# Kernel optimization log

Measured on AMD Instinct MI355X. Metric: run time of the kernel, lower is better.

The kernel has to match this reference:

```python
import jax, jax.numpy as jnp
import numpy as np

PARENT_LIST = [0, 0, 1, 2, 3, 4, 5, 6, 7, 8, 8, 3, 11, 12, 13, 14, 15, 15, 0, 18, 19, 20, 0, 22, 23, 24, 3]
J, D, H, L, DFF = 27, 512, 8, 6, 2048
DH = D // H
RADIUS = 0.1
B, N = 64, 2048
NEG = -1e9  # large finite negative: exp underflows to exactly 0 in fp32, grad-safe


def _topo_mask():
    m = np.full((J, J), NEG, dtype=np.float32)
    for c, p in enumerate(PARENT_LIST):
        m[c, c] = 0.0
        if c != p:
            m[c, p] = 0.0
            m[p, c] = 0.0
    return jnp.asarray(m)


def _radius_scales():
    s = np.ones(J, dtype=np.float32)
    s[[0, 1, 2, 3, 18, 22]] = 0.6
    s[[9, 10, 16, 17, 20, 21, 24, 25, 26]] = 1.5
    return jnp.asarray(s).reshape(1, J, 1)


def _ln(x, s, b):
    mu = jnp.mean(x, -1, keepdims=True)
    v = jnp.mean((x - mu) ** 2, -1, keepdims=True)
    return (x - mu) * jax.lax.rsqrt(v + 1e-5) * s + b


def _mha(q_in, k_in, v_in, qkv_w, qkv_b, out_w, out_b, add_mask):
    Bq, Q, _ = q_in.shape
    S = k_in.shape[1]
    q = (q_in @ qkv_w[:, :D] + qkv_b[:D]).reshape(Bq, Q, H, DH)
    k = (k_in @ qkv_w[:, D:2 * D] + qkv_b[D:2 * D]).reshape(Bq, S, H, DH)
    v = (v_in @ qkv_w[:, 2 * D:] + qkv_b[2 * D:]).reshape(Bq, S, H, DH)
    scores = jnp.einsum('bqhd,bkhd->bhqk', q, k) * np.float32(1.0 / np.sqrt(DH))
    attn = jax.nn.softmax(scores + add_mask, axis=-1)
    o = jnp.einsum('bhqk,bkhd->bqhd', attn, v).reshape(Bq, Q, D)
    return o @ out_w + out_b


def setup_inputs() -> dict:
    key = jax.random.key(0)
    ks = iter(jax.random.split(key, 40))
    def w(shape, scale=0.02):
        return jax.random.normal(next(ks), shape, jnp.float32) * scale
    return dict(
        x_t=jax.random.normal(next(ks), (B, J, 3), jnp.float32),
        t=jax.random.uniform(next(ks), (B, 1), jnp.float32),
        coarse_pose=jax.random.normal(next(ks), (B, J, 3), jnp.float32),
        radar_pc=jax.random.normal(next(ks), (B, N, 6), jnp.float32),
        pc_w=w((6, D)), pc_b=jnp.zeros(D),
        coarse_w=w((3, D)), coarse_b=jnp.zeros(D),
        state_w=w((3, D)), state_b=jnp.zeros(D),
        jid_emb=w((J, D), 1.0),
        dop_w1=w((1, 64)), dop_b1=jnp.zeros(64),
        dop_w2=w((64, D)), dop_b2=jnp.zeros(D),
        time_w1=w((1, D)), time_b1=jnp.zeros(D),
        time_w2=w((D, D)), time_b2=jnp.zeros(D),
        mod_w1=w((D, 2 * D)), mod_b1=jnp.zeros(2 * D),
        mod_w2=w((2 * D, 2 * D)), mod_b2=jnp.zeros(2 * D),
        diff_w=w((2 * D, D)), diff_b=jnp.zeros(D),
        vel_w=w((D, 3)), vel_b=jnp.zeros(3),
        sa_qkv_w=w((L, D, 3 * D)), sa_qkv_b=jnp.zeros((L, 3 * D)),
        sa_out_w=w((L, D, D)), sa_out_b=jnp.zeros((L, D)),
        ca_qkv_w=w((L, D, 3 * D)), ca_qkv_b=jnp.zeros((L, 3 * D)),
        ca_out_w=w((L, D, D)), ca_out_b=jnp.zeros((L, D)),
        ff1_w=w((L, D, DFF)), ff1_b=jnp.zeros((L, DFF)),
        ff2_w=w((L, DFF, D)), ff2_b=jnp.zeros((L, D)),
        ln1_s=jnp.ones((L, D)), ln1_b=jnp.zeros((L, D)),
        ln2_s=jnp.ones((L, D)), ln2_b=jnp.zeros((L, D)),
        ln3_s=jnp.ones((L, D)), ln3_b=jnp.zeros((L, D)),
    )


def reference(x_t, t, coarse_pose, radar_pc, pc_w, pc_b, coarse_w, coarse_b,
              state_w, state_b, jid_emb, dop_w1, dop_b1, dop_w2, dop_b2,
              time_w1, time_b1, time_w2, time_b2, mod_w1, mod_b1, mod_w2, mod_b2,
              diff_w, diff_b, vel_w, vel_b,
              sa_qkv_w, sa_qkv_b, sa_out_w, sa_out_b,
              ca_qkv_w, ca_qkv_b, ca_out_w, ca_out_b,
              ff1_w, ff1_b, ff2_w, ff2_b,
              ln1_s, ln1_b, ln2_s, ln2_b, ln3_s, ln3_b):
    p_idx = jnp.asarray(PARENT_LIST)
    topo = _topo_mask()          # [J,J] additive
    scales = _radius_scales()    # [1,J,1]
    pc_xyz = radar_pc[:, :, :3]
    pc_dop = radar_pc[:, :, 3:4]
    raw_memory = radar_pc @ pc_w + pc_b                               # [B,N,D]
    # euclidean distance via norm expansion (cdist p=2)
    d2 = (jnp.sum(x_t ** 2, -1)[:, :, None] + jnp.sum(pc_xyz ** 2, -1)[:, None, :]
          - 2.0 * jnp.einsum('bjc,bnc->bjn', x_t, pc_xyz))
    dist = jnp.sqrt(jnp.maximum(d2, 0.0))                             # [B,J,N]
    ar = scales * RADIUS                                              # [1,J,1]
    sig = ar / 2.0
    dw = jnp.exp(-dist ** 2 / (2.0 * sig ** 2))                       # [B,J,N]
    pi = jnp.max(dw, axis=1, keepdims=True)                           # [B,1,N]
    memory = raw_memory * jnp.swapaxes(pi, 1, 2)                      # [B,N,D]
    dop_feat = jax.nn.silu(pc_dop @ dop_w1 + dop_b1) @ dop_w2 + dop_b2
    denom = jnp.sum(dw, -1, keepdims=True) + 1e-6
    h_dop = jnp.einsum('bjn,bnd->bjd', dw, dop_feat) / denom
    h_coarse = coarse_pose @ coarse_w + coarse_b
    h_time = (jax.nn.silu(t @ time_w1 + time_b1) @ time_w2 + time_b2)[:, None, :]
    h_state = x_t @ state_w + state_b
    h_parent = h_state[:, p_idx, :]
    h_struct = jnp.concatenate([h_state, h_parent], -1) @ diff_w + diff_b
    query = h_coarse + h_time + h_dop + h_state + h_struct + jid_emb[None]
    mod = jax.nn.silu(h_state @ mod_w1 + mod_b1) @ mod_w2 + mod_b2
    shift, scale = jnp.split(mod, 2, axis=-1)
    query = query * (1.0 + scale) + shift
    # radius mask with nearest-point rescue
    smask = dist > ar
    min_idx = jnp.argmin(dist, axis=-1)                               # [B,J]
    rescue = jnp.arange(dist.shape[-1])[None, None, :] != min_idx[:, :, None]
    smask = jnp.where(jnp.all(smask, -1, keepdims=True), rescue, smask)
    mem_bias = jnp.where(smask, NEG, 0.0)[:, None, :, :]              # [B,1,J,N]
    tgt_bias = topo[None, None]                                       # [1,1,J,J]
    x = query
    for l in range(L):  # norm_first TransformerDecoderLayer, relu FFN, no dropout
        h = _ln(x, ln1_s[l], ln1_b[l])
        x = x + _mha(h, h, h, sa_qkv_w[l], sa_qkv_b[l], sa_out_w[l], sa_out_b[l], tgt_bias)
        h = _ln(x, ln2_s[l], ln2_b[l])
        x = x + _mha(h, memory, memory, ca_qkv_w[l], ca_qkv_b[l], ca_out_w[l], ca_out_b[l], mem_bias)
        h = _ln(x, ln3_s[l], ln3_b[l])
        x = x + jax.nn.relu(h @ ff1_w[l] + ff1_b[l]) @ ff2_w[l] + ff2_b[l]
    return x @ vel_w + vel_b
```

## Files before the change

kernel.cpp:

```cpp
#include <hip/hip_runtime.h>

#define J 27
#define D 512
#define H 8
#define DH 64
#define NLAYER 6
#define DFF 2048
#define NB 64
#define NP 2048
#define CAP 128
#define GCH 16
#define GPTS 128
#define NEGF -1000000000.0f

typedef unsigned short u16;
typedef __attribute__((ext_vector_type(8))) __bf16 bf16x8;
typedef __attribute__((ext_vector_type(4))) float f32x4;

__constant__ int c_parent[J] = {0,0,1,2,3,4,5,6,7,8,8,3,11,12,13,14,15,15,0,18,19,20,0,22,23,24,3};
__constant__ float c_scale[J] = {0.6f,0.6f,0.6f,0.6f,1.f,1.f,1.f,1.f,1.f,1.5f,1.5f,1.f,1.f,1.f,1.f,1.f,
                                 1.5f,1.5f,0.6f,1.f,1.5f,1.5f,0.6f,1.f,1.5f,1.5f,1.5f};

__device__ __forceinline__ float siluf(float x){ return x/(1.f+expf(-x)); }

// ... 173 lines not shown
                        const float* __restrict__ dop_b2, const float* __restrict__ denom_sum,
                        float* __restrict__ h_dop){
  int b = blockIdx.x, half = blockIdx.y;
  int t = threadIdx.x;
  int d = half*256 + t;
  __shared__ float sG[J*64];
  __shared__ float sS[J], sI[J];
  for (int e = t; e < J*64; e += 256){
    float s = 0.f;
    #pragma unroll
    for (int c = 0; c < GCH; ++c) s += Gp[(size_t)(b*GCH+c)*J*64 + e];
    sG[e] = s;
  }
  if (t < J){ float S = denom_sum[b*J+t]; sS[t] = S; sI[t] = 1.f/(S+1e-6f); }
  __syncthreads();
  float acc[J];
  #pragma unroll
  for (int j = 0; j < J; ++j) acc[j] = 0.f;
  for (int h = 0; h < 64; ++h){
    float wv = dop_w2[h*D + d];
    #pragma unroll
    for (int j = 0; j < J; ++j) acc[j] += sG[j*64+h]*wv;
  }
  float b2 = dop_b2[d];
  #pragma unroll
  for (int j = 0; j < J; ++j)
    h_dop[(size_t)(b*J+j)*D + d] = (acc[j] + sS[j]*b2)*sI[j];
}

__global__ void k_stage1(const float* __restrict__ x_t, const float* __restrict__ state_w,
                         const float* __restrict__ state_b,
                         const float* __restrict__ coarse, const float* __restrict__ coarse_w,
                         const float* __restrict__ coarse_b,
                         const float* __restrict__ t_in, const float* __restrict__ time_w1,
                         const float* __restrict__ time_b1,
                         float* __restrict__ h_state, u16* __restrict__ hsh,
                         float* __restrict__ h_coarse, u16* __restrict__ thh,
                         u16* __restrict__ hs2h){
  const int RD = NB*J*D;
  int idx = blockIdx.x*256 + threadIdx.x;
  if (idx < RD){
    int r = idx / D, d = idx % D;
    const float* ir = x_t + r*3;
    float v = ir[0]*state_w[d] + ir[1]*state_w[D+d] + ir[2]*state_w[2*D+d] + state_b[d];
    h_state[idx] = v;
    hsh[idx] = f2bf(v);
  } else if (idx < 2*RD){
    int k = idx - RD;
    int r = k / D, d = k % D;
    const float* ir = coarse + r*3;
    h_coarse[k] = ir[0]*coarse_w[d] + ir[1]*coarse_w[D+d] + ir[2]*coarse_w[2*D+d] + coarse_b[d];
  } else if (idx < 2*RD + NB*D){
    int k = idx - 2*RD;
    int b = k / D, d = k % D;
    float v = siluf(t_in[b]*time_w1[d] + time_b1[d]);
    thh[k] = f2bf(v);
  } else if (idx < 4*RD + NB*D){
    int k = idx - (2*RD + NB*D);
    int r = k / (2*D), c = k % (2*D);
    int b = r / J, j = r % J;
    int src = (c < D) ? r : (b*J + c_parent[j]);
    int d = (c < D) ? c : c - D;
    const float* ir = x_t + src*3;
    float v = ir[0]*state_w[d] + ir[1]*state_w[D+d] + ir[2]*state_w[2*D+d] + state_b[d];
    hs2h[k] = f2bf(v);
  }
}

__global__ void k_query(const float* __restrict__ h_coarse, const float* __restrict__ h_time,
                        const float* __restrict__ h_dop, const float* __restrict__ h_state,
                        const float* __restrict__ hstruct, const float* __restrict__ jid,
                        const float* __restrict__ mod2, float* __restrict__ x){
  int idx = blockIdx.x*256 + threadIdx.x;
  if (idx >= NB*J*D) return;
  int r = idx / D, d = idx % D;
  int b = r / J, j = r % J;
  float q = h_coarse[idx] + h_time[b*D+d] + h_dop[idx] + h_state[idx] + hstruct[idx] + jid[j*D+d];
  float shift = mod2[(size_t)r*2*D + d];
  float scale = mod2[(size_t)r*2*D + D + d];
  x[idx] = q*(1.f+scale) + shift;
}

__global__ void k_memact(const float* __restrict__ x_t, const float* __restrict__ pc,
                         const float* __restrict__ pc_w, const float* __restrict__ pc_b,
                         const int* __restrict__ act_idx, const int* __restrict__ act_cnt,
                         const int* __restrict__ act_off, u16* __restrict__ mh){
  int b = blockIdx.x / CAP, i = blockIdx.x % CAP;
  if (i >= act_cnt[b]) return;
  int n = act_idx[b*CAP+i];
  int t = threadIdx.x;
  __shared__ float sdw[J];
  __shared__ float spi;
  const float* p = pc + ((size_t)b*NP+n)*6;
  if (t < J){
    float x0 = x_t[(b*J+t)*3+0], x1 = x_t[(b*J+t)*3+1], x2 = x_t[(b*J+t)*3+2];
    float p0=p[0], p1=p[1], p2=p[2];
    float d2 = (x0*x0+x1*x1+x2*x2) + (p0*p0+p1*p1+p2*p2) - 2.f*(x0*p0+x1*p1+x2*p2);
    float dist = sqrtf(fmaxf(d2,0.f));
    float sig = c_scale[t]*0.05f;
    sdw[t] = expf(-(dist*dist)/(2.f*sig*sig));
  }
  __syncthreads();
  if (t == 0){ float m = sdw[0]; for (int k = 1; k < J; ++k) m = fmaxf(m, sdw[k]); spi = m; }
  __syncthreads();
  float pi = spi;
  float p0=p[0],p1=p[1],p2=p[2],p3=p[3],p4=p[4],p5=p[5];
  int g = act_off[b] + i;
  for (int d = t; d < D; d += 128){
    float acc = pc_b[d] + p0*pc_w[d] + p1*pc_w[D+d] + p2*pc_w[2*D+d]
              + p3*pc_w[3*D+d] + p4*pc_w[4*D+d] + p5*pc_w[5*D+d];
    mh[(size_t)g*D + d] = f2bf(acc * pi);
  }
}

struct WcD { const float* src; u16* dst; int K; int N; int tk; int tn; int L; int start; };
struct WcTab { WcD d[10]; };
__launch_bounds__(256)
__global__ void k_wconv_all(WcTab tab){
  int tid = blockIdx.x;
  WcD w = tab.d[0];
  #pragma unroll
  for (int i = 0; i < 10; ++i){
    int end = tab.d[i].start + tab.d[i].tk*tab.d[i].tn*tab.d[i].L;
    if (tid >= tab.d[i].start && tid < end) w = tab.d[i];
  }
  int local = tid - w.start;
  int per = w.tk*w.tn;
  int l = local / per, rem = local % per;
  int k0 = (rem % w.tk)*64, n0 = (rem / w.tk)*64;
  size_t zo = (size_t)l*w.K*w.N;
  __shared__ float tile[64][65];
  int t = threadIdx.x;
  #pragma unroll
  for (int i = 0; i < 4; ++i){
    int lin = i*256 + t;
    int k = lin >> 4, nc = lin & 15;
    float4 v = *(const float4*)&w.src[zo + (size_t)(k0+k)*w.N + n0 + nc*4];
    tile[k][nc*4+0]=v.x; tile[k][nc*4+1]=v.y; tile[k][nc*4+2]=v.z; tile[k][nc*4+3]=v.w;
  }
  __syncthreads();
  #pragma unroll
  for (int i = 0; i < 2; ++i){
    int lin = i*256 + t;
    int n = lin >> 3, kc = lin & 7;
    unsigned pk[4];
    #pragma unroll
    for (int u = 0; u < 4; ++u)
      pk[u] = (unsigned)f2bf(tile[kc*8+2*u][n]) | ((unsigned)f2bf(tile[kc*8+2*u+1][n])<<16);
    *(uint4*)&w.dst[zo + (size_t)(n0+n)*w.K + k0 + kc*8] = make_uint4(pk[0],pk[1],pk[2],pk[3]);
  }
}

struct GemmArgs {
  const u16* Ag; const u16* Bt; const float* bias; const float* res;
  float* Cf; u16* Ch; int M, N, K, act; const int* Mdev; int ntx; int nwg;
};

template<int TM>
__device__ __forceinline__ void gemm_body(const GemmArgs g, int bid, char* smem){
  int Meff = g.Mdev ? *g.Mdev : g.M;
  int q8 = g.nwg>>3, r8 = g.nwg&7;
  int xcd = bid&7, loc = bid>>3;
  int wg = (xcd < r8 ? xcd*(q8+1) : r8*(q8+1)+(xcd-r8)*q8) + loc;
  int row0 = (wg % g.ntx)*TM, col0 = (wg / g.ntx)*64;
  if (row0 >= Meff) return;
  char* sA = smem;
  char* sB = smem + TM*64*2;
  int t = threadIdx.x;
  int lane = t&63, w = t>>6, wr = w>>1, wc = w&1;
  int sm = t>>3, kc = t&7;
  int K = g.K, N = g.N;
  const u16* pA1 = g.Ag + (size_t)(row0+sm)*K + kc*8;
  const u16* pA2 = (TM==64) ? g.Ag + (size_t)(row0+sm+32)*K + kc*8 : pA1;
  const u16* pB1 = g.Bt + (size_t)(col0+sm)*K + kc*8;
  const u16* pB2 = g.Bt + (size_t)(col0+sm+32)*K + kc*8;
  int o1 = (sm*128 + kc*16) ^ ((sm&7)<<4);
  int o2 = ((sm+32)*128 + kc*16) ^ ((sm&7)<<4);
  uint4 ra1, ra2, rb1, rb2;
  auto gload = [&](int kt){
    ra1 = *(const uint4*)(pA1 + kt);
    if constexpr (TM==64) ra2 = *(const uint4*)(pA2 + kt);
    rb1 = *(const uint4*)(pB1 + kt);
    rb2 = *(const uint4*)(pB2 + kt);
  };
  auto stage = [&](){
    *(uint4*)(sA + o1) = ra1;
    if constexpr (TM==64) *(uint4*)(sA + o2) = ra2;
    *(uint4*)(sB + o1) = rb1;
    *(uint4*)(sB + o2) = rb2;
  };
  constexpr int MFR = TM/32;
  constexpr int RW  = TM/2;
  int fr = lane&15, fkb = (lane>>4)*16;
  f32x4 acc[MFR][2] = {};
  gload(0);
  stage();
  __syncthreads();
  for (int kt = 0; kt < K; kt += 64){
    bool nxt = kt + 64 < K;
    if (nxt) gload(kt + 64);
    #pragma unroll
    for (int kk = 0; kk < 2; ++kk){
      bf16x8 af[MFR], bf[2];
      #pragma unroll
      for (int m = 0; m < MFR; ++m){
        int row = wr*RW + m*16 + fr;
        int adr = (row*128 + kk*64 + fkb) ^ ((row&7)<<4);
        af[m] = *(const bf16x8*)(sA + adr);
      }
      #pragma unroll
      for (int n = 0; n < 2; ++n){
        int rowb = wc*32 + n*16 + fr;
        int adr = (rowb*128 + kk*64 + fkb) ^ ((rowb&7)<<4);
        bf[n] = *(const bf16x8*)(sB + adr);
      }
      #pragma unroll
      for (int m = 0; m < MFR; ++m)
        #pragma unroll
        for (int n = 0; n < 2; ++n)
          acc[m][n] = __builtin_amdgcn_mfma_f32_16x16x32_bf16(af[m], bf[n], acc[m][n], 0,0,0);
    }
    if (nxt){
      __syncthreads();
      stage();
      __syncthreads();
    }
  }
  int er = (lane>>4)*4, ec = lane&15;
  #pragma unroll
  for (int m = 0; m < MFR; ++m){
    #pragma unroll
    for (int qq = 0; qq < 4; ++qq){
      int r = row0 + wr*RW + m*16 + er + qq;
      if (r >= Meff) continue;
      #pragma unroll
      for (int n = 0; n < 2; ++n){
        int c = col0 + wc*32 + n*16 + ec;
        float v = acc[m][n][qq] + g.bias[c];
        if (g.res) v += g.res[(size_t)r*N + c];
        if (g.act == 1) v = v/(1.f+expf(-v));
        else if (g.act == 2) v = fmaxf(v, 0.f);
        if (g.Cf) g.Cf[(size_t)r*N + c] = v;
        if (g.Ch) g.Ch[(size_t)r*N + c] = f2bf(v);
      }
    }
  }
}

template<int TM>
__launch_bounds__(256)
__global__ void k_gemm(GemmArgs g){
  __shared__ __align__(16) char smem[TM*64*2 + 64*64*2];
  gemm_body<TM>(g, blockIdx.x, smem);
}

template<int TMA, int TMB>
__launch_bounds__(256)
__global__ void k_gemm_dual(GemmArgs ga, GemmArgs gb){
  constexpr int SA = TMA*64*2 + 64*64*2;
  constexpr int SB = TMB*64*2 + 64*64*2;
  constexpr int SZ = SA > SB ? SA : SB;
  __shared__ __align__(16) char smem[SZ];
  if ((int)blockIdx.x < ga.nwg) gemm_body<TMA>(ga, blockIdx.x, smem);
  else                          gemm_body<TMB>(gb, blockIdx.x - ga.nwg, smem);
}

__global__ void k_ln(const float* __restrict__ x, const float* __restrict__ s,
                     const float* __restrict__ bb, u16* __restrict__ oh){
  int r = blockIdx.x; int t = threadIdx.x;
  const float* xr = x + (size_t)r*D;
  float v0 = xr[t], v1 = xr[t+256];
  __shared__ float red[256];
  red[t] = v0+v1; __syncthreads();
  for (int st = 128; st > 0; st >>= 1){ if (t < st) red[t] += red[t+st]; __syncthreads(); }
  float mu = red[0]/(float)D;
  __syncthreads();
  float d0 = v0-mu, d1 = v1-mu;
  red[t] = d0*d0 + d1*d1; __syncthreads();
  for (int st = 128; st > 0; st >>= 1){ if (t < st) red[t] += red[t+st]; __syncthreads(); }
  float var = red[0]/(float)D;
  float rs = rsqrtf(var + 1e-5f);
  oh[(size_t)r*D + t]       = f2bf(d0*rs*s[t]       + bb[t]);
  oh[(size_t)r*D + t + 256] = f2bf(d1*rs*s[t+256]   + bb[t+256]);
}

__launch_bounds__(256)
__global__ void k_selfattn(const float* __restrict__ qkv, u16* __restrict__ oh){
  int bh = blockIdx.x; int b = bh / H, h = bh % H;
  int t = threadIdx.x;
  __shared__ float qs[J*DH], ks[J*DH], vs[J*DH];
  __shared__ float ss[J*J];
  for (int e = t; e < J*DH; e += 256){
    int j = e/DH, d = e%DH;
    const float* base = qkv + (size_t)(b*J+j)*1536 + h*DH + d;
    qs[e] = base[0]; ks[e] = base[512]; vs[e] = base[1024];
  }
  __syncthreads();
  for (int e = t; e < J*J; e += 256){
    int qj = e/J, kk = e%J;
    float acc = 0.f;
    for (int d = 0; d < DH; ++d) acc += qs[qj*DH+d]*ks[kk*DH+d];
    float bias = (qj==kk || c_parent[qj]==kk || c_parent[kk]==qj) ? 0.f : NEGF;
    ss[e] = acc*0.125f + bias;
  }
  __syncthreads();
  if (t < J){
    float m = -3.4e38f;
    for (int k = 0; k < J; ++k) m = fmaxf(m, ss[t*J+k]);
    float sum = 0.f;
    for (int k = 0; k < J; ++k){ float e_ = expf(ss[t*J+k]-m); ss[t*J+k] = e_; sum += e_; }
    float inv = 1.f/sum;
    for (int k = 0; k < J; ++k) ss[t*J+k] *= inv;
  }
  __syncthreads();
  for (int e = t; e < J*DH; e += 256){
    int j = e/DH, d = e%DH;
    float acc = 0.f;
    for (int k = 0; k < J; ++k) acc += ss[j*J+k]*vs[k*DH+d];
    oh[(size_t)(b*J+j)*D + h*DH + d] = f2bf(acc);
  }
}

__launch_bounds__(256)
__global__ void k_crossattn(const float* __restrict__ qbuf, const float* __restrict__ kv_act,
                            const float* __restrict__ x_t, const float* __restrict__ pc,
                            const int* __restrict__ act_idx, const int* __restrict__ act_cnt,
                            const int* __restrict__ act_off, const int* __restrict__ rescue,
                            const int* __restrict__ allm, u16* __restrict__ oh){
  int bh = blockIdx.x; int b = bh / H, h = bh % H;
  int t = threadIdx.x;
  int cnt = act_cnt[b], off = act_off[b];
  __shared__ float qs[J*DH];
  __shared__ float ks[CAP*DH];
  __shared__ float pxyz[CAP*3];
  __shared__ float sx[J*3];
  __shared__ int sn[CAP];
  __shared__ float ss[J*CAP];
  if (t < J*3) sx[t] = x_t[b*J*3+t];
  for (int e = t; e < J*DH; e += 256)
    qs[e] = qbuf[(size_t)(b*J + e/DH)*D + h*DH + (e%DH)];
  for (int e = t; e < cnt*DH; e += 256){
    int i = e/DH, d = e%DH;
    ks[e] = kv_act[(size_t)(off+i)*1024 + h*DH + d];
  }
  for (int i = t; i < cnt; i += 256){
    int n = act_idx[b*CAP+i]; sn[i] = n;
    const float* p = pc + ((size_t)b*NP+n)*6;
    pxyz[i*3] = p[0]; pxyz[i*3+1] = p[1]; pxyz[i*3+2] = p[2];
  }
  __syncthreads();
  for (int e = t; e < J*cnt; e += 256){
    int j = e/cnt, i = e%cnt;
    float acc = 0.f;
    for (int d = 0; d < DH; ++d) acc += qs[j*DH+d]*ks[i*DH+d];
    float bias;
    if (allm[b*J+j]) bias = (sn[i] == rescue[b*J+j]) ? 0.f : NEGF;
    else {
      float x0=sx[j*3], x1=sx[j*3+1], x2=sx[j*3+2];
      float p0=pxyz[i*3], p1=pxyz[i*3+1], p2=pxyz[i*3+2];
      float d2 = (x0*x0+x1*x1+x2*x2) + (p0*p0+p1*p1+p2*p2) - 2.f*(x0*p0+x1*p1+x2*p2);
      float dist = sqrtf(fmaxf(d2,0.f));
      float ar = c_scale[j]*0.1f;
      bias = (dist > ar) ? NEGF : 0.f;
    }
    ss[j*CAP+i] = acc*0.125f + bias;
  }
  __syncthreads();
  if (t < J){
    float m = -3.4e38f;
    for (int i = 0; i < cnt; ++i) m = fmaxf(m, ss[t*CAP+i]);
    float sum = 0.f;
    for (int i = 0; i < cnt; ++i){ float e_ = expf(ss[t*CAP+i]-m); ss[t*CAP+i] = e_; sum += e_; }
    float inv = 1.f/sum;
    for (int i = 0; i < cnt; ++i) ss[t*CAP+i] *= inv;
  }
  __syncthreads();
  for (int e = t; e < J*DH; e += 256){
    int j = e/DH, d = e%DH;
    float acc = 0.f;
    for (int i = 0; i < cnt; ++i)
      acc += ss[j*CAP+i]*kv_act[(size_t)(off+i)*1024 + 512 + h*DH + d];
    oh[(size_t)(b*J+j)*D + h*DH + d] = f2bf(acc);
  }
}

__global__ void k_vel(const float* __restrict__ x, const float* __restrict__ vel_w,
                      const float* __restrict__ vel_b, float* __restrict__ out){
  int r = blockIdx.x; int t = threadIdx.x;
  int c = t >> 6; int lane = t & 63;
  float acc = 0.f;
  const float* xr = x + (size_t)r*D;
  for (int d = lane; d < D; d += 64) acc += xr[d]*vel_w[d*3+c];
  for (int s = 32; s > 0; s >>= 1) acc += __shfl_down(acc, s);
  if (lane == 0) out[r*3+c] = acc + vel_b[c];
}

static GemmArgs mk(const u16* A, const u16* Bt, const float* bias, const float* res,
                   float* Cf, u16* Ch, int M, int N, int K, int act, const int* Mdev, int TM){
  GemmArgs g; g.Ag=A; g.Bt=Bt; g.bias=bias; g.res=res; g.Cf=Cf; g.Ch=Ch;
  g.M=M; g.N=N; g.K=K; g.act=act; g.Mdev=Mdev;
  g.ntx=(M+TM-1)/TM; g.nwg=g.ntx*(N/64); return g;
}

extern "C" void kernel_launch(void* const* d_in, const int* in_sizes, int n_in,
                              void* d_out, int out_size, void* d_ws, size_t ws_size,
                              hipStream_t stream){
  const float* x_t        = (const float*)d_in[0];
  const float* t_in       = (const float*)d_in[1];
  const float* coarse     = (const float*)d_in[2];
  const float* radar      = (const float*)d_in[3];
  const float* pc_w       = (const float*)d_in[4];
  const float* pc_b       = (const float*)d_in[5];
  const float* coarse_w   = (const float*)d_in[6];
  const float* coarse_b   = (const float*)d_in[7];
  const float* state_w    = (const float*)d_in[8];
  const float* state_b    = (const float*)d_in[9];
  const float* jid_emb    = (const float*)d_in[10];
  const float* dop_w1     = (const float*)d_in[11];
  const float* dop_b1     = (const float*)d_in[12];
  const float* dop_w2     = (const float*)d_in[13];
  const float* dop_b2     = (const float*)d_in[14];
  const float* time_w1    = (const float*)d_in[15];
  const float* time_b1    = (const float*)d_in[16];
  const float* time_w2    = (const float*)d_in[17];
  const float* time_b2    = (const float*)d_in[18];
  const float* mod_w1     = (const float*)d_in[19];
  const float* mod_b1     = (const float*)d_in[20];
  const float* mod_w2     = (const float*)d_in[21];
  const float* mod_b2     = (const float*)d_in[22];
  const float* diff_w     = (const float*)d_in[23];
  const float* diff_b     = (const float*)d_in[24];
  const float* vel_w      = (const float*)d_in[25];
  const float* vel_b      = (const float*)d_in[26];
  const float* sa_qkv_w   = (const float*)d_in[27];
  const float* sa_qkv_b   = (const float*)d_in[28];
  const float* sa_out_w   = (const float*)d_in[29];
  const float* sa_out_b   = (const float*)d_in[30];
  const float* ca_qkv_w   = (const float*)d_in[31];
  const float* ca_qkv_b   = (const float*)d_in[32];
  const float* ca_out_w   = (const float*)d_in[33];
  const float* ca_out_b   = (const float*)d_in[34];
  const float* ff1_w      = (const float*)d_in[35];
  const float* ff1_b      = (const float*)d_in[36];
  const float* ff2_w      = (const float*)d_in[37];
  const float* ff2_b      = (const float*)d_in[38];
  const float* ln1_s      = (const float*)d_in[39];
  const float* ln1_b      = (const float*)d_in[40];
  const float* ln2_s      = (const float*)d_in[41];
  const float* ln2_b      = (const float*)d_in[42];
  const float* ln3_s      = (const float*)d_in[43];
  const float* ln3_b      = (const float*)d_in[44];
  (void)in_sizes; (void)n_in; (void)out_size; (void)ws_size;

  const int R = NB*J;

  char* wp = (char*)d_ws;
  auto alloc = [&](size_t bytes)->void*{
    void* r = (void*)wp;
    wp += (bytes + 255) & ~(size_t)255;
    return r;
  };
  float*        denom_sum = (float*)alloc(R*4);
  int*          rescue    = (int*)  alloc(R*4);
  int*          allm      = (int*)  alloc(R*4);
  unsigned int* bitmap    = (unsigned int*)alloc(NB*(NP/32)*4);
  int*          act_idx   = (int*)  alloc(NB*CAP*4);
  int*          act_cnt   = (int*)  alloc(NB*4);
  int*          act_off   = (int*)  alloc(NB*4);
  int*          act_total = (int*)  alloc(64);
  float* Gp       = (float*)alloc((size_t)NB*GCH*J*64*4);
  float* h_dop    = (float*)alloc((size_t)R*D*4);
  float* h_state  = (float*)alloc((size_t)R*D*4);
  float* h_coarse = (float*)alloc((size_t)R*D*4);
  float* hstruct  = (float*)alloc((size_t)R*D*4);
  float* xres     = (float*)alloc((size_t)R*D*4);
  float* qbuf     = (float*)alloc((size_t)R*D*4);
  float* h_time   = (float*)alloc((size_t)NB*D*4);
  float* mod2     = (float*)alloc((size_t)R*2*D*4);
  float* qkv      = (float*)alloc((size_t)R*3*D*4);
  float* kv_act   = (float*)alloc((size_t)NB*CAP*2*D*4);
  u16* hsh   = (u16*)alloc((size_t)R*D*2);
  u16* hbufh = (u16*)alloc((size_t)R*D*2);
  u16* attnoh= (u16*)alloc((size_t)R*D*2);
  u16* ffhh  = (u16*)alloc((size_t)R*DFF*2);
  u16* mah   = (u16*)alloc((size_t)NB*CAP*D*2);
  u16* time_w2t = (u16*)alloc((size_t)512*512*2);
  u16* mod_w1t  = (u16*)alloc((size_t)1024*512*2);
  u16* mod_w2t  = (u16*)alloc((size_t)1024*1024*2);
  u16* diff_wt  = (u16*)alloc((size_t)512*1024*2);
  u16* sa_qkv_t = (u16*)alloc((size_t)NLAYER*1536*512*2);
  u16* sa_out_t = (u16*)alloc((size_t)NLAYER*512*512*2);
  u16* ca_qkv_t = (u16*)alloc((size_t)NLAYER*1536*512*2);
  u16* ca_out_t = (u16*)alloc((size_t)NLAYER*512*512*2);
  u16* ff1_t    = (u16*)alloc((size_t)NLAYER*2048*512*2);
  u16* ff2_t    = (u16*)alloc((size_t)NLAYER*512*2048*2);
  u16* thh   = attnoh;
  u16* mod1h = ffhh;
  u16* hs2h  = (u16*)kv_act;

  {
    WcTab tab;
    int s = 0;
    auto set = [&](int i, const float* src, u16* dst, int K, int N, int L){
      tab.d[i].src = src; tab.d[i].dst = dst; tab.d[i].K = K; tab.d[i].N = N;
      tab.d[i].tk = K/64; tab.d[i].tn = N/64; tab.d[i].L = L; tab.d[i].start = s;
      s += (K/64)*(N/64)*L;
    };
    set(0, time_w2, time_w2t, 512, 512, 1);
    set(1, mod_w1,  mod_w1t,  512, 1024, 1);
    set(2, mod_w2,  mod_w2t,  1024, 1024, 1);
    set(3, diff_w,  diff_wt,  1024, 512, 1);
    set(4, sa_qkv_w, sa_qkv_t, 512, 1536, NLAYER);
    set(5, sa_out_w, sa_out_t, 512, 512, NLAYER);
    set(6, ca_qkv_w, ca_qkv_t, 512, 1536, NLAYER);
    set(7, ca_out_w, ca_out_t, 512, 512, NLAYER);
    set(8, ff1_w,    ff1_t,    512, 2048, NLAYER);
    set(9, ff2_w,    ff2_t,    2048, 512, NLAYER);
    k_wconv_all<<<s, 256, 0, stream>>>(tab);
  }

  hipMemsetAsync(bitmap, 0, NB*(NP/32)*4, stream);
  k_perj<<<R, 256, 0, stream>>>(x_t, radar, denom_sum, rescue, allm, bitmap);
  k_compact<<<1, 1024, 0, stream>>>(bitmap, act_idx, act_cnt, act_off, act_total);
  k_gpart<<<dim3(NB, GCH), 256, 0, stream>>>(x_t, radar, dop_w1, dop_b1, Gp);
  k_hdop2<<<dim3(NB, 2), 256, 0, stream>>>(Gp, dop_w2, dop_b2, denom_sum, h_dop);

  k_stage1<<<(4*R*D + NB*D + 255)/256, 256, 0, stream>>>(
      x_t, state_w, state_b, coarse, coarse_w, coarse_b, t_in, time_w1, time_b1,
      h_state, hsh, h_coarse, thh, hs2h);
  { GemmArgs ga = mk(thh, time_w2t, time_b2, nullptr, h_time, nullptr, NB, 512, 512, 0, nullptr, 32);
    GemmArgs gb = mk(hsh, mod_w1t, mod_b1, nullptr, nullptr, mod1h, R, 1024, 512, 1, nullptr, 32);
    k_gemm_dual<32,32><<<ga.nwg + gb.nwg, 256, 0, stream>>>(ga, gb); }
  { GemmArgs ga = mk(mod1h, mod_w2t, mod_b2, nullptr, mod2, nullptr, R, 1024, 1024, 0, nullptr, 32);
    GemmArgs gb = mk(hs2h, diff_wt, diff_b, nullptr, hstruct, nullptr, R, 512, 1024, 0, nullptr, 32);
    k_gemm_dual<32,32><<<ga.nwg + gb.nwg, 256, 0, stream>>>(ga, gb); }
  k_query<<<(R*D+255)/256, 256, 0, stream>>>(h_coarse, h_time, h_dop, h_state, hstruct,
                                             jid_emb, mod2, xres);
  k_memact<<<NB*CAP, 128, 0, stream>>>(x_t, radar, pc_w, pc_b, act_idx, act_cnt, act_off, mah);

  for (int l = 0; l < NLAYER; ++l){
    k_ln<<<R, 256, 0, stream>>>(xres, ln1_s + l*D, ln1_b + l*D, hbufh);
    { GemmArgs g = mk(hbufh, sa_qkv_t + (size_t)l*1536*512, sa_qkv_b + l*1536, nullptr,
                      qkv, nullptr, R, 1536, 512, 0, nullptr, 32);
      k_gemm<32><<<g.nwg, 256, 0, stream>>>(g); }
    k_selfattn<<<NB*H, 256, 0, stream>>>(qkv, attnoh);
    { GemmArgs g = mk(attnoh, sa_out_t + (size_t)l*512*512, sa_out_b + l*D, xres,
                      xres, nullptr, R, 512, 512, 0, nullptr, 32);
      k_gemm<32><<<g.nwg, 256, 0, stream>>>(g); }

    k_ln<<<R, 256, 0, stream>>>(xres, ln2_s + l*D, ln2_b + l*D, hbufh);
    { GemmArgs ga = mk(hbufh, ca_qkv_t + (size_t)l*1536*512, ca_qkv_b + l*1536, nullptr,
                       qbuf, nullptr, R, 512, 512, 0, nullptr, 32);
      GemmArgs gb = mk(mah, ca_qkv_t + (size_t)l*1536*512 + (size_t)512*512,
                       ca_qkv_b + l*1536 + 512, nullptr,
                       kv_act, nullptr, NB*CAP, 1024, 512, 0, act_total, 64);
      k_gemm_dual<32,64><<<ga.nwg + gb.nwg, 256, 0, stream>>>(ga, gb); }
    k_crossattn<<<NB*H, 256, 0, stream>>>(qbuf, kv_act, x_t, radar, act_idx, act_cnt,
                                          act_off, rescue, allm, attnoh);
    { GemmArgs g = mk(attnoh, ca_out_t + (size_t)l*512*512, ca_out_b + l*D, xres,
                      xres, nullptr, R, 512, 512, 0, nullptr, 32);
      k_gemm<32><<<g.nwg, 256, 0, stream>>>(g); }

    k_ln<<<R, 256, 0, stream>>>(xres, ln3_s + l*D, ln3_b + l*D, hbufh);
    { GemmArgs g = mk(hbufh, ff1_t + (size_t)l*2048*512, ff1_b + l*DFF, nullptr,
                      nullptr, ffhh, R, 2048, 512, 2, nullptr, 32);
      k_gemm<32><<<g.nwg, 256, 0, stream>>>(g); }
    { GemmArgs g = mk(ffhh, ff2_t + (size_t)l*512*2048, ff2_b + l*D, xres,
                      xres, nullptr, R, 512, 2048, 0, nullptr, 32);
      k_gemm<32><<<g.nwg, 256, 0, stream>>>(g); }
  }

  k_vel<<<R, 192, 0, stream>>>(xres, vel_w, vel_b, (float*)d_out);
}
```

Measured before the change: 1.001 ms.

## Fuse LayerNorm into GEMM A-operand staging and regroup cross-attn KV GEMM

Removes the standalone LayerNorm kernels. Each GEMM workgroup now computes per-row mean and rstd from the fp32 residual and applies scale and shift while converting A tiles to bf16 in shared memory. The cross-attention KV projection, which depends only on memory, now runs in the same dual launch as the self-attention QKV GEMM, so the launch count per layer drops. In exchange, every column tile recomputes the row statistics and reads fp32 A instead of bf16, which raises redundant global traffic.

```diff
diff --git a/kernel.cpp b/kernel.cpp
--- a/kernel.cpp
+++ b/kernel.cpp
@@ -349,11 +349,13 @@
 }
 
 struct GemmArgs {
-  const u16* Ag; const u16* Bt; const float* bias; const float* res;
+  const u16* Ag; const float* Af; const u16* Bt;
+  const float* bias; const float* res;
+  const float* lnS; const float* lnB;
   float* Cf; u16* Ch; int M, N, K, act; const int* Mdev; int ntx; int nwg;
 };
 
-template<int TM>
+template<int TM, bool LN>
 __device__ __forceinline__ void gemm_body(const GemmArgs g, int bid, char* smem){
   int Meff = g.Mdev ? *g.Mdev : g.M;
   int q8 = g.nwg>>3, r8 = g.nwg&7;
@@ -363,26 +365,101 @@
   if (row0 >= Meff) return;
   char* sA = smem;
   char* sB = smem + TM*64*2;
+  float* smu = (float*)(smem + TM*64*2 + 64*64*2);
+  float* srs = smu + TM;
   int t = threadIdx.x;
   int lane = t&63, w = t>>6, wr = w>>1, wc = w&1;
   int sm = t>>3, kc = t&7;
   int K = g.K, N = g.N;
-  const u16* pA1 = g.Ag + (size_t)(row0+sm)*K + kc*8;
-  const u16* pA2 = (TM==64) ? g.Ag + (size_t)(row0+sm+32)*K + kc*8 : pA1;
+
+  if constexpr (LN){
+    int lr = t & 7, rr = t >> 3;
+    #pragma unroll
+    for (int rb = 0; rb < TM; rb += 32){
+      int row = rb + rr;
+      int grow = row0 + row;
+      float mu = 0.f, rs = 0.f;
+      if (grow < g.M){
+        const float* xr = g.Af + (size_t)grow*K + lr*(K/8);
+        int cnt = K/8;
+        float s = 0.f;
+        for (int i = 0; i < cnt; i += 4){
+          float4 v = *(const float4*)(xr + i);
+          s += v.x + v.y + v.z + v.w;
+        }
+        s += __shfl_xor(s,1); s += __shfl_xor(s,2); s += __shfl_xor(s,4);
+        mu = s/(float)K;
+        float vs = 0.f;
+        for (int i = 0; i < cnt; i += 4){
+          float4 v = *(const float4*)(xr + i);
+          float d0=v.x-mu, d1=v.y-mu, d2=v.z-mu, d3=v.w-mu;
+          vs += d0*d0 + d1*d1 + d2*d2 + d3*d3;
+        }
+        vs += __shfl_xor(vs,1); vs += __shfl_xor(vs,2); vs += __shfl_xor(vs,4);
+        rs = rsqrtf(vs/(float)K + 1e-5f);
+      }
+      if (lr == 0){ smu[row] = mu; srs[row] = rs; }
+    }
+    __syncthreads();
+  }
+
+  const u16* pA1 = nullptr; const u16* pA2 = nullptr;
+  const float* pAf1 = nullptr; const float* pAf2 = nullptr;
+  if constexpr (LN){
+    pAf1 = g.Af + (size_t)(row0+sm)*K + kc*8;
+    if constexpr (TM==64) pAf2 = g.Af + (size_t)(row0+sm+32)*K + kc*8;
+  } else {
+    pA1 = g.Ag + (size_t)(row0+sm)*K + kc*8;
+    if constexpr (TM==64) pA2 = g.Ag + (size_t)(row0+sm+32)*K + kc*8;
+  }
   const u16* pB1 = g.Bt + (size_t)(col0+sm)*K + kc*8;
   const u16* pB2 = g.Bt + (size_t)(col0+sm+32)*K + kc*8;
   int o1 = (sm*128 + kc*16) ^ ((sm&7)<<4);
   int o2 = ((sm+32)*128 + kc*16) ^ ((sm&7)<<4);
   uint4 ra1, ra2, rb1, rb2;
+  float fa1[8], fa2[8];
   auto gload = [&](int kt){
-    ra1 = *(const uint4*)(pA1 + kt);
-    if constexpr (TM==64) ra2 = *(const uint4*)(pA2 + kt);
+    if constexpr (LN){
+      *(float4*)&fa1[0] = *(const float4*)(pAf1 + kt);
+      *(float4*)&fa1[4] = *(const float4*)(pAf1 + kt + 4);
+      if constexpr (TM==64){
+        *(float4*)&fa2[0] = *(const float4*)(pAf2 + kt);
+        *(float4*)&fa2[4] = *(const float4*)(pAf2 + kt + 4);
+      }
+    } else {
+      ra1 = *(const uint4*)(pA1 + kt);
+      if constexpr (TM==64) ra2 = *(const uint4*)(pA2 + kt);
+    }
     rb1 = *(const uint4*)(pB1 + kt);
     rb2 = *(const uint4*)(pB2 + kt);
   };
-  auto stage = [&](){
-    *(uint4*)(sA + o1) = ra1;
-    if constexpr (TM==64) *(uint4*)(sA + o2) = ra2;
+  auto stage = [&](int kt){
+    if constexpr (LN){
+      float mu = smu[sm], rs = srs[sm];
+      const float* Sv = g.lnS + kt + kc*8;
+      const float* Bv = g.lnB + kt + kc*8;
+      unsigned pk[4];
+      #pragma unroll
+      for (int u = 0; u < 4; ++u){
+        float y0 = (fa1[2*u]  -mu)*rs*Sv[2*u]   + Bv[2*u];
+        float y1 = (fa1[2*u+1]-mu)*rs*Sv[2*u+1] + Bv[2*u+1];
+        pk[u] = (unsigned)f2bf(y0) | ((unsigned)f2bf(y1)<<16);
+      }
+      *(uint4*)(sA + o1) = make_uint4(pk[0],pk[1],pk[2],pk[3]);
+      if constexpr (TM==64){
+        float mu2 = smu[sm+32], rs2 = srs[sm+32];
+        #pragma unroll
+        for (int u = 0; u < 4; ++u){
+          float y0 = (fa2[2*u]  -mu2)*rs2*Sv[2*u]   + Bv[2*u];
+          float y1 = (fa2[2*u+1]-mu2)*rs2*Sv[2*u+1] + Bv[2*u+1];
+          pk[u] = (unsigned)f2bf(y0) | ((unsigned)f2bf(y1)<<16);
+        }
+        *(uint4*)(sA + o2) = make_uint4(pk[0],pk[1],pk[2],pk[3]);
+      }
+    } else {
+      *(uint4*)(sA + o1) = ra1;
+      if constexpr (TM==64) *(uint4*)(sA + o2) = ra2;
+    }
     *(uint4*)(sB + o1) = rb1;
     *(uint4*)(sB + o2) = rb2;
   };
@@ -391,7 +468,7 @@
   int fr = lane&15, fkb = (lane>>4)*16;
   f32x4 acc[MFR][2] = {};
   gload(0);
-  stage();
+  stage(0);
   __syncthreads();
   for (int kt = 0; kt < K; kt += 64){
     bool nxt = kt + 64 < K;
@@ -419,7 +496,7 @@
     }
     if (nxt){
       __syncthreads();
-      stage();
+      stage(kt + 64);
       __syncthreads();
     }
   }
@@ -444,41 +521,23 @@
   }
 }
 
-template<int TM>
+template<int TM, bool LN>
 __launch_bounds__(256)
 __global__ void k_gemm(GemmArgs g){
-  __shared__ __align__(16) char smem[TM*64*2 + 64*64*2];
-  gemm_body<TM>(g, blockIdx.x, smem);
-}
-
-template<int TMA, int TMB>
+  constexpr int SZ = TM*64*2 + 64*64*2 + TM*8;
+  __shared__ __align__(16) char smem[SZ];
+  gemm_body<TM,LN>(g, blockIdx.x, smem);
+}
+
+template<int TMA, bool LNA, int TMB, bool LNB>
 __launch_bounds__(256)
 __global__ void k_gemm_dual(GemmArgs ga, GemmArgs gb){
-  constexpr int SA = TMA*64*2 + 64*64*2;
-  constexpr int SB = TMB*64*2 + 64*64*2;
+  constexpr int SA = TMA*64*2 + 64*64*2 + TMA*8;
+  constexpr int SB = TMB*64*2 + 64*64*2 + TMB*8;
   constexpr int SZ = SA > SB ? SA : SB;
   __shared__ __align__(16) char smem[SZ];
-  if ((int)blockIdx.x < ga.nwg) gemm_body<TMA>(ga, blockIdx.x, smem);
-  else                          gemm_body<TMB>(gb, blockIdx.x - ga.nwg, smem);
-}
-
-__global__ void k_ln(const float* __restrict__ x, const float* __restrict__ s,
-                     const float* __restrict__ bb, u16* __restrict__ oh){
-  int r = blockIdx.x; int t = threadIdx.x;
-  const float* xr = x + (size_t)r*D;
-  float v0 = xr[t], v1 = xr[t+256];
-  __shared__ float red[256];
-  red[t] = v0+v1; __syncthreads();
-  for (int st = 128; st > 0; st >>= 1){ if (t < st) red[t] += red[t+st]; __syncthreads(); }
-  float mu = red[0]/(float)D;
-  __syncthreads();
-  float d0 = v0-mu, d1 = v1-mu;
-  red[t] = d0*d0 + d1*d1; __syncthreads();
-  for (int st = 128; st > 0; st >>= 1){ if (t < st) red[t] += red[t+st]; __syncthreads(); }
-  float var = red[0]/(float)D;
-  float rs = rsqrtf(var + 1e-5f);
-  oh[(size_t)r*D + t]       = f2bf(d0*rs*s[t]       + bb[t]);
-  oh[(size_t)r*D + t + 256] = f2bf(d1*rs*s[t+256]   + bb[t+256]);
+  if ((int)blockIdx.x < ga.nwg) gemm_body<TMA,LNA>(ga, blockIdx.x, smem);
+  else                          gemm_body<TMB,LNB>(gb, blockIdx.x - ga.nwg, smem);
 }
 
 __launch_bounds__(256)
@@ -594,8 +653,17 @@
 
 static GemmArgs mk(const u16* A, const u16* Bt, const float* bias, const float* res,
                    float* Cf, u16* Ch, int M, int N, int K, int act, const int* Mdev, int TM){
-  GemmArgs g; g.Ag=A; g.Bt=Bt; g.bias=bias; g.res=res; g.Cf=Cf; g.Ch=Ch;
+  GemmArgs g; g.Ag=A; g.Af=nullptr; g.Bt=Bt; g.bias=bias; g.res=res;
+  g.lnS=nullptr; g.lnB=nullptr; g.Cf=Cf; g.Ch=Ch;
   g.M=M; g.N=N; g.K=K; g.act=act; g.Mdev=Mdev;
+  g.ntx=(M+TM-1)/TM; g.nwg=g.ntx*(N/64); return g;
+}
+static GemmArgs mkLN(const float* Af, const float* lnS, const float* lnB,
+                     const u16* Bt, const float* bias, const float* res,
+                     float* Cf, u16* Ch, int M, int N, int K, int act, int TM){
+  GemmArgs g; g.Ag=nullptr; g.Af=Af; g.Bt=Bt; g.bias=bias; g.res=res;
+  g.lnS=lnS; g.lnB=lnB; g.Cf=Cf; g.Ch=Ch;
+  g.M=M; g.N=N; g.K=K; g.act=act; g.Mdev=nullptr;
   g.ntx=(M+TM-1)/TM; g.nwg=g.ntx*(N/64); return g;
 }
 
@@ -677,7 +745,6 @@
   float* qkv      = (float*)alloc((size_t)R*3*D*4);
   float* kv_act   = (float*)alloc((size_t)NB*CAP*2*D*4);
   u16* hsh   = (u16*)alloc((size_t)R*D*2);
-  u16* hbufh = (u16*)alloc((size_t)R*D*2);
   u16* attnoh= (u16*)alloc((size_t)R*D*2);
   u16* ffhh  = (u16*)alloc((size_t)R*DFF*2);
   u16* mah   = (u16*)alloc((size_t)NB*CAP*D*2);
@@ -727,44 +794,44 @@
       h_state, hsh, h_coarse, thh, hs2h);
   { GemmArgs ga = mk(thh, time_w2t, time_b2, nullptr, h_time, nullptr, NB, 512, 512, 0, nullptr, 32);
     GemmArgs gb = mk(hsh, mod_w1t, mod_b1, nullptr, nullptr, mod1h, R, 1024, 512, 1, nullptr, 32);
-    k_gemm_dual<32,32><<<ga.nwg + gb.nwg, 256, 0, stream>>>(ga, gb); }
+    k_gemm_dual<32,false,32,false><<<ga.nwg + gb.nwg, 256, 0, stream>>>(ga, gb); }
   { GemmArgs ga = mk(mod1h, mod_w2t, mod_b2, nullptr, mod2, nullptr, R, 1024, 1024, 0, nullptr, 32);
     GemmArgs gb = mk(hs2h, diff_wt, diff_b, nullptr, hstruct, nullptr, R, 512, 1024, 0, nullptr, 32);
-    k_gemm_dual<32,32><<<ga.nwg + gb.nwg, 256, 0, stream>>>(ga, gb); }
+    k_gemm_dual<32,false,32,false><<<ga.nwg + gb.nwg, 256, 0, stream>>>(ga, gb); }
   k_query<<<(R*D+255)/256, 256, 0, stream>>>(h_coarse, h_time, h_dop, h_state, hstruct,
                                              jid_emb, mod2, xres);
   k_memact<<<NB*CAP, 128, 0, stream>>>(x_t, radar, pc_w, pc_b, act_idx, act_cnt, act_off, mah);
 
   for (int l = 0; l < NLAYER; ++l){
-    k_ln<<<R, 256, 0, stream>>>(xres, ln1_s + l*D, ln1_b + l*D, hbufh);
-    { GemmArgs g = mk(hbufh, sa_qkv_t + (size_t)l*1536*512, sa_qkv_b + l*1536, nullptr,
-                      qkv, nullptr, R, 1536, 512, 0, nullptr, 32);
-      k_gemm<32><<<g.nwg, 256, 0, stream>>>(g); }
+    { GemmArgs ga = mkLN(xres, ln1_s + l*D, ln1_b + l*D,
+                         sa_qkv_t + (size_t)l*1536*512, sa_qkv_b + l*1536, nullptr,
+                         qkv, nullptr, R, 1536, 512, 0, 32);
+      GemmArgs gb = mk(mah, ca_qkv_t + (size_t)l*1536*512 + (size_t)512*512,
+                       ca_qkv_b + l*1536 + 512, nullptr,
+                       kv_act, nullptr, NB*CAP, 1024, 512, 0, act_total, 64);
+      k_gemm_dual<32,true,64,false><<<ga.nwg + gb.nwg, 256, 0, stream>>>(ga, gb); }
     k_selfattn<<<NB*H, 256, 0, stream>>>(qkv, attnoh);
     { GemmArgs g = mk(attnoh, sa_out_t + (size_t)l*512*512, sa_out_b + l*D, xres,
                       xres, nullptr, R, 512, 512, 0, nullptr, 32);
-      k_gemm<32><<<g.nwg, 256, 0, stream>>>(g); }
-
-    k_ln<<<R, 256, 0, stream>>>(xres, ln2_s + l*D, ln2_b + l*D, hbufh);
-    { GemmArgs ga = mk(hbufh, ca_qkv_t + (size_t)l*1536*512, ca_qkv_b + l*1536, nullptr,
-                       qbuf, nullptr, R, 512, 512, 0, nullptr, 32);
-      GemmArgs gb = mk(mah, ca_qkv_t + (size_t)l*1536*512 + (size_t)512*512,
-                       ca_qkv_b + l*1536 + 512, nullptr,
-                       kv_act, nullptr, NB*CAP, 1024, 512, 0, act_total, 64);
-      k_gemm_dual<32,64><<<ga.nwg + gb.nwg, 256, 0, stream>>>(ga, gb); }
+      k_gemm<32,false><<<g.nwg, 256, 0, stream>>>(g); }
+
+    { GemmArgs g = mkLN(xres, ln2_s + l*D, ln2_b + l*D,
+                        ca_qkv_t + (size_t)l*1536*512, ca_qkv_b + l*1536, nullptr,
+                        qbuf, nullptr, R, 512, 512, 0, 32);
+      k_gemm<32,true><<<g.nwg, 256, 0, stream>>>(g); }
     k_crossattn<<<NB*H, 256, 0, stream>>>(qbuf, kv_act, x_t, radar, act_idx, act_cnt,
                                           act_off, rescue, allm, attnoh);
     { GemmArgs g = mk(attnoh, ca_out_t + (size_t)l*512*512, ca_out_b + l*D, xres,
                       xres, nullptr, R, 512, 512, 0, nullptr, 32);
-      k_gemm<32><<<g.nwg, 256, 0, stream>>>(g); }
-
-    k_ln<<<R, 256, 0, stream>>>(xres, ln3_s + l*D, ln3_b + l*D, hbufh);
-    { GemmArgs g = mk(hbufh, ff1_t + (size_t)l*2048*512, ff1_b + l*DFF, nullptr,
-                      nullptr, ffhh, R, 2048, 512, 2, nullptr, 32);
-      k_gemm<32><<<g.nwg, 256, 0, stream>>>(g); }
+      k_gemm<32,false><<<g.nwg, 256, 0, stream>>>(g); }
+
+    { GemmArgs g = mkLN(xres, ln3_s + l*D, ln3_b + l*D,
+                        ff1_t + (size_t)l*2048*512, ff1_b + l*DFF, nullptr,
+                        nullptr, ffhh, R, 2048, 512, 2, 32);
+      k_gemm<32,true><<<g.nwg, 256, 0, stream>>>(g); }
     { GemmArgs g = mk(ffhh, ff2_t + (size_t)l*512*2048, ff2_b + l*D, xres,
                       xres, nullptr, R, 512, 2048, 0, nullptr, 32);
-      k_gemm<32><<<g.nwg, 256, 0, stream>>>(g); }
+      k_gemm<32,false><<<g.nwg, 256, 0, stream>>>(g); }
   }
 
   k_vel<<<R, 192, 0, stream>>>(xres, vel_w, vel_b, (float*)d_out);
```

New measurement: 1.724 ms. 1.72x slower.

## Add N-tile template parameter and move cross-attn KV GEMM into self-attn QKV launch

Applied to the files above, without the earlier changes.

Generalises the GEMM body to a configurable N tile (64 or 128) with the warp layout derived from it, and uses 32x128 tiles for the wider GEMMs (QKV, FF1, mod projections) to raise reuse of the A tile. The memory K/V projection for cross-attention does not depend on the residual stream, so it is now launched together with the self-attention QKV GEMM in one dual kernel. The cross-attention Q projection becomes a standalone launch. Wider tiles mean fewer workgroups and more registers per thread, which may lower occupancy and parallelism at M=1728.

```diff
diff --git a/kernel.cpp b/kernel.cpp
--- a/kernel.cpp
+++ b/kernel.cpp
@@ -353,41 +353,48 @@
   float* Cf; u16* Ch; int M, N, K, act; const int* Mdev; int ntx; int nwg;
 };
 
-template<int TM>
+template<int TM, int TN>
 __device__ __forceinline__ void gemm_body(const GemmArgs g, int bid, char* smem){
   int Meff = g.Mdev ? *g.Mdev : g.M;
   int q8 = g.nwg>>3, r8 = g.nwg&7;
   int xcd = bid&7, loc = bid>>3;
   int wg = (xcd < r8 ? xcd*(q8+1) : r8*(q8+1)+(xcd-r8)*q8) + loc;
-  int row0 = (wg % g.ntx)*TM, col0 = (wg / g.ntx)*64;
+  int row0 = (wg % g.ntx)*TM, col0 = (wg / g.ntx)*TN;
   if (row0 >= Meff) return;
+  constexpr int WC  = TN/32;
+  constexpr int WR  = 4/WC;
+  constexpr int RPW = TM/WR;
+  constexpr int MFR = RPW/16;
+  constexpr int AR  = TM/32;
+  constexpr int BR  = TN/32;
   char* sA = smem;
   char* sB = smem + TM*64*2;
   int t = threadIdx.x;
-  int lane = t&63, w = t>>6, wr = w>>1, wc = w&1;
+  int lane = t&63, w = t>>6;
+  int wr = w / WC, wc = w % WC;
   int sm = t>>3, kc = t&7;
   int K = g.K, N = g.N;
-  const u16* pA1 = g.Ag + (size_t)(row0+sm)*K + kc*8;
-  const u16* pA2 = (TM==64) ? g.Ag + (size_t)(row0+sm+32)*K + kc*8 : pA1;
-  const u16* pB1 = g.Bt + (size_t)(col0+sm)*K + kc*8;
-  const u16* pB2 = g.Bt + (size_t)(col0+sm+32)*K + kc*8;
-  int o1 = (sm*128 + kc*16) ^ ((sm&7)<<4);
-  int o2 = ((sm+32)*128 + kc*16) ^ ((sm&7)<<4);
-  uint4 ra1, ra2, rb1, rb2;
+  const u16* pA[2]; const u16* pB[4];
+  int oo[4];
+  #pragma unroll
+  for (int r = 0; r < AR; ++r) pA[r] = g.Ag + (size_t)(row0+sm+32*r)*K + kc*8;
+  #pragma unroll
+  for (int r = 0; r < BR; ++r) pB[r] = g.Bt + (size_t)(col0+sm+32*r)*K + kc*8;
+  #pragma unroll
+  for (int r = 0; r < 4; ++r) oo[r] = ((sm+32*r)*128 + kc*16) ^ ((sm&7)<<4);
+  uint4 ra[2], rb[4];
   auto gload = [&](int kt){
-    ra1 = *(const uint4*)(pA1 + kt);
-    if constexpr (TM==64) ra2 = *(const uint4*)(pA2 + kt);
-    rb1 = *(const uint4*)(pB1 + kt);
-    rb2 = *(const uint4*)(pB2 + kt);
+    #pragma unroll
+    for (int r = 0; r < AR; ++r) ra[r] = *(const uint4*)(pA[r] + kt);
+    #pragma unroll
+    for (int r = 0; r < BR; ++r) rb[r] = *(const uint4*)(pB[r] + kt);
   };
   auto stage = [&](){
-    *(uint4*)(sA + o1) = ra1;
-    if constexpr (TM==64) *(uint4*)(sA + o2) = ra2;
-    *(uint4*)(sB + o1) = rb1;
-    *(uint4*)(sB + o2) = rb2;
+    #pragma unroll
+    for (int r = 0; r < AR; ++r) *(uint4*)(sA + oo[r]) = ra[r];
+    #pragma unroll
+    for (int r = 0; r < BR; ++r) *(uint4*)(sB + oo[r]) = rb[r];
   };
-  constexpr int MFR = TM/32;
-  constexpr int RW  = TM/2;
   int fr = lane&15, fkb = (lane>>4)*16;
   f32x4 acc[MFR][2] = {};
   gload(0);
@@ -401,7 +408,7 @@
       bf16x8 af[MFR], bf[2];
       #pragma unroll
       for (int m = 0; m < MFR; ++m){
-        int row = wr*RW + m*16 + fr;
+        int row = wr*RPW + m*16 + fr;
         int adr = (row*128 + kk*64 + fkb) ^ ((row&7)<<4);
         af[m] = *(const bf16x8*)(sA + adr);
       }
@@ -428,7 +435,7 @@
   for (int m = 0; m < MFR; ++m){
     #pragma unroll
     for (int qq = 0; qq < 4; ++qq){
-      int r = row0 + wr*RW + m*16 + er + qq;
+      int r = row0 + wr*RPW + m*16 + er + qq;
       if (r >= Meff) continue;
       #pragma unroll
       for (int n = 0; n < 2; ++n){
@@ -444,22 +451,22 @@
   }
 }
 
-template<int TM>
+template<int TM, int TN>
 __launch_bounds__(256)
 __global__ void k_gemm(GemmArgs g){
-  __shared__ __align__(16) char smem[TM*64*2 + 64*64*2];
-  gemm_body<TM>(g, blockIdx.x, smem);
-}
-
-template<int TMA, int TMB>
+  __shared__ __align__(16) char smem[(TM+TN)*64*2];
+  gemm_body<TM,TN>(g, blockIdx.x, smem);
+}
+
+template<int TMA, int TNA, int TMB, int TNB>
 __launch_bounds__(256)
 __global__ void k_gemm_dual(GemmArgs ga, GemmArgs gb){
-  constexpr int SA = TMA*64*2 + 64*64*2;
-  constexpr int SB = TMB*64*2 + 64*64*2;
+  constexpr int SA = (TMA+TNA)*64*2;
+  constexpr int SB = (TMB+TNB)*64*2;
   constexpr int SZ = SA > SB ? SA : SB;
   __shared__ __align__(16) char smem[SZ];
-  if ((int)blockIdx.x < ga.nwg) gemm_body<TMA>(ga, blockIdx.x, smem);
-  else                          gemm_body<TMB>(gb, blockIdx.x - ga.nwg, smem);
+  if ((int)blockIdx.x < ga.nwg) gemm_body<TMA,TNA>(ga, blockIdx.x, smem);
+  else                          gemm_body<TMB,TNB>(gb, blockIdx.x - ga.nwg, smem);
 }
 
 __global__ void k_ln(const float* __restrict__ x, const float* __restrict__ s,
@@ -593,10 +600,11 @@
 }
 
 static GemmArgs mk(const u16* A, const u16* Bt, const float* bias, const float* res,
-                   float* Cf, u16* Ch, int M, int N, int K, int act, const int* Mdev, int TM){
+                   float* Cf, u16* Ch, int M, int N, int K, int act, const int* Mdev,
+                   int TM, int TN){
   GemmArgs g; g.Ag=A; g.Bt=Bt; g.bias=bias; g.res=res; g.Cf=Cf; g.Ch=Ch;
   g.M=M; g.N=N; g.K=K; g.act=act; g.Mdev=Mdev;
-  g.ntx=(M+TM-1)/TM; g.nwg=g.ntx*(N/64); return g;
+  g.ntx=(M+TM-1)/TM; g.nwg=g.ntx*(N/TN); return g;
 }
 
 extern "C" void kernel_launch(void* const* d_in, const int* in_sizes, int n_in,
@@ -725,46 +733,46 @@
   k_stage1<<<(4*R*D + NB*D + 255)/256, 256, 0, stream>>>(
       x_t, state_w, state_b, coarse, coarse_w, coarse_b, t_in, time_w1, time_b1,
       h_state, hsh, h_coarse, thh, hs2h);
-  { GemmArgs ga = mk(thh, time_w2t, time_b2, nullptr, h_time, nullptr, NB, 512, 512, 0, nullptr, 32);
-    GemmArgs gb = mk(hsh, mod_w1t, mod_b1, nullptr, nullptr, mod1h, R, 1024, 512, 1, nullptr, 32);
-    k_gemm_dual<32,32><<<ga.nwg + gb.nwg, 256, 0, stream>>>(ga, gb); }
-  { GemmArgs ga = mk(mod1h, mod_w2t, mod_b2, nullptr, mod2, nullptr, R, 1024, 1024, 0, nullptr, 32);
-    GemmArgs gb = mk(hs2h, diff_wt, diff_b, nullptr, hstruct, nullptr, R, 512, 1024, 0, nullptr, 32);
-    k_gemm_dual<32,32><<<ga.nwg + gb.nwg, 256, 0, stream>>>(ga, gb); }
+  { GemmArgs ga = mk(thh, time_w2t, time_b2, nullptr, h_time, nullptr, NB, 512, 512, 0, nullptr, 32, 64);
+    GemmArgs gb = mk(hsh, mod_w1t, mod_b1, nullptr, nullptr, mod1h, R, 1024, 512, 1, nullptr, 32, 128);
+    k_gemm_dual<32,64,32,128><<<ga.nwg + gb.nwg, 256, 0, stream>>>(ga, gb); }
+  { GemmArgs ga = mk(mod1h, mod_w2t, mod_b2, nullptr, mod2, nullptr, R, 1024, 1024, 0, nullptr, 32, 128);
+    GemmArgs gb = mk(hs2h, diff_wt, diff_b, nullptr, hstruct, nullptr, R, 512, 1024, 0, nullptr, 32, 64);
+    k_gemm_dual<32,128,32,64><<<ga.nwg + gb.nwg, 256, 0, stream>>>(ga, gb); }
   k_query<<<(R*D+255)/256, 256, 0, stream>>>(h_coarse, h_time, h_dop, h_state, hstruct,
                                              jid_emb, mod2, xres);
   k_memact<<<NB*CAP, 128, 0, stream>>>(x_t, radar, pc_w, pc_b, act_idx, act_cnt, act_off, mah);
 
   for (int l = 0; l < NLAYER; ++l){
     k_ln<<<R, 256, 0, stream>>>(xres, ln1_s + l*D, ln1_b + l*D, hbufh);
-    { GemmArgs g = mk(hbufh, sa_qkv_t + (size_t)l*1536*512, sa_qkv_b + l*1536, nullptr,
-                      qkv, nullptr, R, 1536, 512, 0, nullptr, 32);
-      k_gemm<32><<<g.nwg, 256, 0, stream>>>(g); }
+    { GemmArgs ga = mk(hbufh, sa_qkv_t + (size_t)l*1536*512, sa_qkv_b + l*1536, nullptr,
+                       qkv, nullptr, R, 1536, 512, 0, nullptr, 32, 128);
+      GemmArgs gb = mk(mah, ca_qkv_t + (size_t)l*1536*512 + (size_t)512*512,
+                       ca_qkv_b + l*1536 + 512, nullptr,
+                       kv_act, nullptr, NB*CAP, 1024, 512, 0, act_total, 64, 64);
+      k_gemm_dual<32,128,64,64><<<ga.nwg + gb.nwg, 256, 0, stream>>>(ga, gb); }
     k_selfattn<<<NB*H, 256, 0, stream>>>(qkv, attnoh);
     { GemmArgs g = mk(attnoh, sa_out_t + (size_t)l*512*512, sa_out_b + l*D, xres,
-                      xres, nullptr, R, 512, 512, 0, nullptr, 32);
-      k_gemm<32><<<g.nwg, 256, 0, stream>>>(g); }
+                      xres, nullptr, R, 512, 512, 0, nullptr, 32, 64);
+      k_gemm<32,64><<<g.nwg, 256, 0, stream>>>(g); }
 
     k_ln<<<R, 256, 0, stream>>>(xres, ln2_s + l*D, ln2_b + l*D, hbufh);
-    { GemmArgs ga = mk(hbufh, ca_qkv_t + (size_t)l*1536*512, ca_qkv_b + l*1536, nullptr,
-                       qbuf, nullptr, R, 512, 512, 0, nullptr, 32);
-      GemmArgs gb = mk(mah, ca_qkv_t + (size_t)l*1536*512 + (size_t)512*512,
-                       ca_qkv_b + l*1536 + 512, nullptr,
-                       kv_act, nullptr, NB*CAP, 1024, 512, 0, act_total, 64);
-      k_gemm_dual<32,64><<<ga.nwg + gb.nwg, 256, 0, stream>>>(ga, gb); }
+    { GemmArgs g = mk(hbufh, ca_qkv_t + (size_t)l*1536*512, ca_qkv_b + l*1536, nullptr,
+                      qbuf, nullptr, R, 512, 512, 0, nullptr, 32, 64);
+      k_gemm<32,64><<<g.nwg, 256, 0, stream>>>(g); }
     k_crossattn<<<NB*H, 256, 0, stream>>>(qbuf, kv_act, x_t, radar, act_idx, act_cnt,
                                           act_off, rescue, allm, attnoh);
     { GemmArgs g = mk(attnoh, ca_out_t + (size_t)l*512*512, ca_out_b + l*D, xres,
-                      xres, nullptr, R, 512, 512, 0, nullptr, 32);
-      k_gemm<32><<<g.nwg, 256, 0, stream>>>(g); }
+                      xres, nullptr, R, 512, 512, 0, nullptr, 32, 64);
+      k_gemm<32,64><<<g.nwg, 256, 0, stream>>>(g); }
 
     k_ln<<<R, 256, 0, stream>>>(xres, ln3_s + l*D, ln3_b + l*D, hbufh);
     { GemmArgs g = mk(hbufh, ff1_t + (size_t)l*2048*512, ff1_b + l*DFF, nullptr,
-                      nullptr, ffhh, R, 2048, 512, 2, nullptr, 32);
-      k_gemm<32><<<g.nwg, 256, 0, stream>>>(g); }
+                      nullptr, ffhh, R, 2048, 512, 2, nullptr, 32, 128);
+      k_gemm<32,128><<<g.nwg, 256, 0, stream>>>(g); }
     { GemmArgs g = mk(ffhh, ff2_t + (size_t)l*512*2048, ff2_b + l*D, xres,
-                      xres, nullptr, R, 512, 2048, 0, nullptr, 32);
-      k_gemm<32><<<g.nwg, 256, 0, stream>>>(g); }
+                      xres, nullptr, R, 512, 2048, 0, nullptr, 32, 64);
+      k_gemm<32,64><<<g.nwg, 256, 0, stream>>>(g); }
   }
 
   k_vel<<<R, 192, 0, stream>>>(xres, vel_w, vel_b, (float*)d_out);
```

Measured after the change: 2.047 ms. 104% more time.
